# Kernel optimization log

Hardware: AMD Instinct MI355X
Metric: run time of the kernel (lower is better)

## Reference

```python
import jax, jax.numpy as jnp
import numpy as np

N_NODES = 50000
N_EDGES = 640000
HIDDEN = 128
LN_EPS = 1e-5


def setup_inputs() -> dict:
    key = jax.random.key(0)
    k_h, k_e, k_w1, k_w2 = jax.random.split(key, 4)
    s = 1.0 / np.sqrt(HIDDEN)
    return {
        "h": jax.random.normal(k_h, (N_NODES, HIDDEN), dtype=jnp.float32),
        "edge_index": jax.random.randint(k_e, (2, N_EDGES), 0, N_NODES, dtype=jnp.int32),
        "W1": jax.random.normal(k_w1, (HIDDEN, HIDDEN), dtype=jnp.float32) * s,
        "b1": jnp.zeros((HIDDEN,), dtype=jnp.float32),
        "W2": jax.random.normal(k_w2, (HIDDEN, HIDDEN), dtype=jnp.float32) * s,
        "b2": jnp.zeros((HIDDEN,), dtype=jnp.float32),
        "eps": jnp.zeros((), dtype=jnp.float32),  # GINConv train_eps init
        "gamma": jnp.ones((HIDDEN,), dtype=jnp.float32),
        "beta": jnp.zeros((HIDDEN,), dtype=jnp.float32),
    }


def reference(h, edge_index, W1, b1, W2, b2, eps, gamma, beta):
    src, dst = edge_index[0], edge_index[1]
    # GIN aggregation: sum of neighbor features scattered to destination nodes
    agg = jax.ops.segment_sum(h[src], dst, num_segments=h.shape[0])  # (N, D)
    z = (1.0 + eps) * h + agg
    # 2-layer MLP: Linear -> ReLU -> Linear (torch Linear: x @ W.T + b)
    z = jax.nn.relu(z @ W1.T + b1)
    h_conv = z @ W2.T + b2
    # residual + LayerNorm + ReLU (dropout is identity in eval mode)
    h_res = h_conv + h
    mu = jnp.mean(h_res, axis=-1, keepdims=True)
    var = jnp.var(h_res, axis=-1, keepdims=True)
    h_norm = (h_res - mu) * jax.lax.rsqrt(var + LN_EPS) * gamma + beta
    return jax.nn.relu(h_norm)
```

## Files before the change

kernel.cpp:

```cpp
#include <hip/hip_runtime.h>

#define HID 128
#define LN_EPS 1e-5f
#define LDSW 136

typedef __attribute__((ext_vector_type(8))) short bf16x8;
typedef __attribute__((ext_vector_type(4))) float f32x4;

static __device__ __forceinline__ unsigned short f2bf(float f) {
  unsigned int x = __float_as_uint(f);
  x += 0x7fffu + ((x >> 16) & 1u);
  return (unsigned short)(x >> 16);
}
static __device__ __forceinline__ float bflo(unsigned int u) { return __uint_as_float(u << 16); }
static __device__ __forceinline__ float bfhi(unsigned int u) { return __uint_as_float(u & 0xffff0000u); }

__global__ __launch_bounds__(256) void k_count(const int* __restrict__ ei,
                                               int* __restrict__ counts, int nE) {
  const int e = blockIdx.x * 256 + threadIdx.x;
  if (e >= nE) return;
  atomicAdd(&counts[ei[nE + e]], 1);
}

__global__ __launch_bounds__(256) void k_scan1(const int* __restrict__ counts,
                                               int* __restrict__ offsets,
                                               int* __restrict__ bsum, int n) {
  __shared__ int sm[256];
  const int t = threadIdx.x;
  const int i = blockIdx.x * 256 + t;
  const int v = (i < n) ? counts[i] : 0;
  int incl = v;
  sm[t] = incl;
  __syncthreads();
#pragma unroll
  for (int off = 1; off < 256; off <<= 1) {
    const int other = (t >= off) ? sm[t - off] : 0;
    __syncthreads();
    incl += other;
    sm[t] = incl;
    __syncthreads();
  }
  if (i < n) offsets[i] = incl - v;
  if (t == 255) bsum[blockIdx.x] = incl;
}

__global__ __launch_bounds__(256) void k_scan2(const int* __restrict__ bsum,
                                               int* __restrict__ ebase,
                                               int* __restrict__ offsets,
                                               int nb, int n) {
  __shared__ int sm[256];
  const int t = threadIdx.x;
  const int v = (t < nb) ? bsum[t] : 0;
  int incl = v;
  sm[t] = incl;
  __syncthreads();
#pragma unroll
  for (int off = 1; off < 256; off <<= 1) {
    const int other = (t >= off) ? sm[t - off] : 0;
    __syncthreads();
    incl += other;
    sm[t] = incl;
    __syncthreads();
  }
  if (t < nb) ebase[t] = incl - v;
  if (t == 255) offsets[n] = incl;
}

__global__ __launch_bounds__(256) void k_scan3(int* __restrict__ offsets,
                                               int* __restrict__ cursors,
                                               const int* __restrict__ ebase, int n) {
  const int i = blockIdx.x * 256 + threadIdx.x;
  if (i >= n) return;
  const int o = offsets[i] + ebase[blockIdx.x];
  offsets[i] = o;
  cursors[i] = o;
}

__global__ __launch_bounds__(256) void k_bucket(const int* __restrict__ ei,
                                                int* __restrict__ cursors,
                                                int* __restrict__ esrc, int nE) {
  const int e = blockIdx.x * 256 + threadIdx.x;
  if (e >= nE) return;
  const int s = ei[e];
  const int d = ei[nE + e];
  const int pos = atomicAdd(&cursors[d], 1);
  esrc[pos] = s;
}

__global__ __launch_bounds__(256) void k_tobf3(const float* __restrict__ h,
                                               const float* __restrict__ w1,
                                               const float* __restrict__ w2,
                                               uint2* __restrict__ hb,
                                               uint2* __restrict__ w1b,
                                               uint2* __restrict__ w2b,
                                               int nh4, int nw4) {
  const int total = nh4 + 2 * nw4;
  const int stride = gridDim.x * 256;
  for (int i = blockIdx.x * 256 + threadIdx.x; i < total; i += stride) {
    const float* src;
    uint2* dst;
    int off;
    if (i < nh4) { src = h; dst = hb; off = i; }
    else if (i < nh4 + nw4) { src = w1; dst = w1b; off = i - nh4; }
    else { src = w2; dst = w2b; off = i - nh4 - nw4; }
    const float4 v = reinterpret_cast<const float4*>(src)[off];
    uint2 p;
    p.x = (unsigned)f2bf(v.x) | ((unsigned)f2bf(v.y) << 16);
    p.y = (unsigned)f2bf(v.z) | ((unsigned)f2bf(v.w) << 16);
    dst[off] = p;
  }
}

__global__ __launch_bounds__(256) void k_gather(const unsigned short* __restrict__ hbf,
                                                const int* __restrict__ offsets,
                                                const int* __restrict__ esrc,
                                                const float* __restrict__ eps,
                                                unsigned short* __restrict__ zbf, int nNodes) {
  const int gid = blockIdx.x * 256 + threadIdx.x;
  const int node = gid >> 5;
  if (node >= nNodes) return;
  const int col4 = (threadIdx.x & 31) * 4;
  const float c = 1.0f + eps[0];

  const uint2 hv = *reinterpret_cast<const uint2*>(hbf + (size_t)node * HID + col4);
  float a0 = c * bflo(hv.x), a1 = c * bfhi(hv.x);
  float a2 = c * bflo(hv.y), a3 = c * bfhi(hv.y);

  const int beg = offsets[node], end = offsets[node + 1];
  int e = beg;
  for (; e + 1 < end; e += 2) {
    const int s0 = esrc[e], s1 = esrc[e + 1];
    const uint2 v0 = *reinterpret_cast<const uint2*>(hbf + (size_t)s0 * HID + col4);
    const uint2 v1 = *reinterpret_cast<const uint2*>(hbf + (size_t)s1 * HID + col4);
    a0 += bflo(v0.x) + bflo(v1.x);
    a1 += bfhi(v0.x) + bfhi(v1.x);
    a2 += bflo(v0.y) + bflo(v1.y);
    a3 += bfhi(v0.y) + bfhi(v1.y);
  }
  if (e < end) {
    const uint2 v0 = *reinterpret_cast<const uint2*>(hbf + (size_t)esrc[e] * HID + col4);
    a0 += bflo(v0.x); a1 += bfhi(v0.x); a2 += bflo(v0.y); a3 += bfhi(v0.y);
  }
  uint2 o;
  o.x = (unsigned)f2bf(a0) | ((unsigned)f2bf(a1) << 16);
  o.y = (unsigned)f2bf(a2) | ((unsigned)f2bf(a3) << 16);
  *reinterpret_cast<uint2*>(zbf + (size_t)node * HID + col4) = o;
}

__global__ __launch_bounds__(256) void k_mmf(const unsigned short* __restrict__ zbf,
                                             const unsigned short* __restrict__ w1,
                                             const unsigned short* __restrict__ w2,
                                             const float* __restrict__ b1,
                                             const float* __restrict__ b2,
                                             const float* __restrict__ h,
                                             const float* __restrict__ gamma,
                                             const float* __restrict__ beta,
                                             float* __restrict__ out, int nTiles) {
  __shared__ unsigned short yt[4][16][LDSW];
  const int wave = threadIdx.x >> 6;
  const int l = threadIdx.x & 63;
  const int mtile = blockIdx.x * 4 + wave;
  if (mtile >= nTiles) return;
  const int row0 = mtile * 16;
  const int lr = l & 15;
  const int lq = l >> 4;

  bf16x8 a[4];
#pragma unroll
  for (int ks = 0; ks < 4; ++ks)
    a[ks] = *reinterpret_cast<const bf16x8*>(zbf + (size_t)(row0 + lr) * HID + ks * 32 + lq * 8);

  f32x4 acc[8];
#pragma unroll
  for (int nt = 0; nt < 8; ++nt) acc[nt] = (f32x4){0.f, 0.f, 0.f, 0.f};
#pragma unroll
  for (int nt = 0; nt < 8; ++nt) {
    const unsigned short* wb = w1 + (size_t)(nt * 16 + lr) * HID + lq * 8;
#pragma unroll
    for (int ks = 0; ks < 4; ++ks) {
      const bf16x8 b = *reinterpret_cast<const bf16x8*>(wb + ks * 32);
      acc[nt] = __builtin_amdgcn_mfma_f32_16x16x32_bf16(a[ks], b, acc[nt], 0, 0, 0);
    }
  }

#pragma unroll
  for (int nt = 0; nt < 8; ++nt) {
    const int cc = nt * 16 + lr;
    const float bs = b1[cc];
#pragma unroll
    for (int r = 0; r < 4; ++r)
      yt[wave][lq * 4 + r][cc] = f2bf(fmaxf(acc[nt][r] + bs, 0.f));
  }

  bf16x8 a2[4];
#pragma unroll
  for (int ks = 0; ks < 4; ++ks)
    a2[ks] = *reinterpret_cast<const bf16x8*>(&yt[wave][lr][ks * 32 + lq * 8]);

#pragma unroll
  for (int nt = 0; nt < 8; ++nt) acc[nt] = (f32x4){0.f, 0.f, 0.f, 0.f};
#pragma unroll
  for (int nt = 0; nt < 8; ++nt) {
    const unsigned short* wb = w2 + (size_t)(nt * 16 + lr) * HID + lq * 8;
#pragma unroll
    for (int ks = 0; ks < 4; ++ks) {
      const bf16x8 b = *reinterpret_cast<const bf16x8*>(wb + ks * 32);
      acc[nt] = __builtin_amdgcn_mfma_f32_16x16x32_bf16(a2[ks], b, acc[nt], 0, 0, 0);
    }
  }

#pragma unroll
  for (int nt = 0; nt < 8; ++nt) {
    const int cc = nt * 16 + lr;
    const float bs = b2[cc];
#pragma unroll
    for (int r = 0; r < 4; ++r) {
      const int row = row0 + lq * 4 + r;
      acc[nt][r] += bs + h[(size_t)row * HID + cc];
    }
  }

  float mu_[4], rstd_[4];
#pragma unroll
  for (int r = 0; r < 4; ++r) {
    float s = 0.f, ss = 0.f;
#pragma unroll
    for (int nt = 0; nt < 8; ++nt) { const float v = acc[nt][r]; s += v; ss += v * v; }
#pragma unroll
    for (int m = 1; m < 16; m <<= 1) {
      s += __shfl_xor(s, m, 64);
      ss += __shfl_xor(ss, m, 64);
    }
    const float mu = s * (1.f / 128.f);
    const float var = ss * (1.f / 128.f) - mu * mu;
    mu_[r] = mu;
    rstd_[r] = rsqrtf(var + LN_EPS);
  }
#pragma unroll
  for (int nt = 0; nt < 8; ++nt) {
    const int cc = nt * 16 + lr;
    const float g = gamma[cc], be = beta[cc];
#pragma unroll
    for (int r = 0; r < 4; ++r) {
      const int row = row0 + lq * 4 + r;
      const float o = (acc[nt][r] - mu_[r]) * rstd_[r] * g + be;
      out[(size_t)row * HID + cc] = fmaxf(o, 0.f);
    }
  }
}

extern "C" void kernel_launch(void* const* d_in, const int* in_sizes, int n_in,
                              void* d_out, int out_size, void* d_ws, size_t ws_size,
                              hipStream_t stream) {
  const float* h     = (const float*)d_in[0];
  const int*   ei    = (const int*)d_in[1];
  const float* W1    = (const float*)d_in[2];
  const float* b1    = (const float*)d_in[3];
  const float* W2    = (const float*)d_in[4];
  const float* b2    = (const float*)d_in[5];
  const float* eps   = (const float*)d_in[6];
  const float* gamma = (const float*)d_in[7];
  const float* beta  = (const float*)d_in[8];

  const int nNodes = in_sizes[0] / HID;
  const int nE     = in_sizes[1] / 2;
  const int nb     = (nNodes + 255) / 256;

  int* counts  = (int*)d_ws;
  int* offsets = counts + nNodes;
  int* cursors = offsets + nNodes + 1;
  int* bsum    = cursors + nNodes;
  int* ebase   = bsum + nb;
  int* esrc    = counts + 150400;
  unsigned short* hbf  = (unsigned short*)(esrc + nE);
  unsigned short* zbf  = hbf + (size_t)nNodes * HID;
  unsigned short* w1bf = zbf + (size_t)nNodes * HID;
  unsigned short* w2bf = w1bf + HID * HID;

  hipMemsetAsync(counts, 0, (size_t)nNodes * sizeof(int), stream);

  const int eblocks = (nE + 255) / 256;
  k_tobf3<<<2048, 256, 0, stream>>>(h, W1, W2, (uint2*)hbf, (uint2*)w1bf, (uint2*)w2bf,
                                    nNodes * HID / 4, HID * HID / 4);
  k_count<<<eblocks, 256, 0, stream>>>(ei, counts, nE);
  k_scan1<<<nb, 256, 0, stream>>>(counts, offsets, bsum, nNodes);
  k_scan2<<<1, 256, 0, stream>>>(bsum, ebase, offsets, nb, nNodes);
  k_scan3<<<nb, 256, 0, stream>>>(offsets, cursors, ebase, nNodes);
  k_bucket<<<eblocks, 256, 0, stream>>>(ei, cursors, esrc, nE);

  k_gather<<<(nNodes * 32 + 255) / 256, 256, 0, stream>>>(hbf, offsets, esrc, eps, zbf, nNodes);

  const int nTiles = nNodes / 16;
  const int mblocks = (nTiles + 3) / 4;
  k_mmf<<<mblocks, 256, 0, stream>>>(zbf, w1bf, w2bf, b1, b2, h, gamma, beta,
                                     (float*)d_out, nTiles);
}
```

Before: 247.8 us.

## Split MLP output columns across four waves per 16-row tile in fused kernel

The fused MLP+LayerNorm kernel previously gave each wave a full 16-row tile covering all 128 output columns. Now a block handles one 16-row tile, and each of its four waves computes 32 output columns. The hidden activation is shared through LDS, and the LayerNorm partial sums are combined across waves with a block barrier. This gives four times as many blocks and fewer accumulator registers per wave, raising occupancy. In exchange, every wave reloads the same A fragment, two __syncthreads are added, and extra LDS traffic is needed for the reduction.

```diff
diff --git a/kernel.cpp b/kernel.cpp
--- a/kernel.cpp
+++ b/kernel.cpp
@@ -156,10 +156,11 @@
                                              const float* __restrict__ gamma,
                                              const float* __restrict__ beta,
                                              float* __restrict__ out, int nTiles) {
-  __shared__ unsigned short yt[4][16][LDSW];
+  __shared__ unsigned short yt[16][LDSW];
+  __shared__ float lnp[16][4][2];
   const int wave = threadIdx.x >> 6;
   const int l = threadIdx.x & 63;
-  const int mtile = blockIdx.x * 4 + wave;
+  const int mtile = blockIdx.x;
   if (mtile >= nTiles) return;
   const int row0 = mtile * 16;
   const int lr = l & 15;
@@ -170,66 +171,85 @@
   for (int ks = 0; ks < 4; ++ks)
     a[ks] = *reinterpret_cast<const bf16x8*>(zbf + (size_t)(row0 + lr) * HID + ks * 32 + lq * 8);
 
-  f32x4 acc[8];
-#pragma unroll
-  for (int nt = 0; nt < 8; ++nt) acc[nt] = (f32x4){0.f, 0.f, 0.f, 0.f};
-#pragma unroll
-  for (int nt = 0; nt < 8; ++nt) {
+  f32x4 acc[2];
+#pragma unroll
+  for (int j = 0; j < 2; ++j) acc[j] = (f32x4){0.f, 0.f, 0.f, 0.f};
+#pragma unroll
+  for (int j = 0; j < 2; ++j) {
+    const int nt = wave * 2 + j;
     const unsigned short* wb = w1 + (size_t)(nt * 16 + lr) * HID + lq * 8;
 #pragma unroll
     for (int ks = 0; ks < 4; ++ks) {
       const bf16x8 b = *reinterpret_cast<const bf16x8*>(wb + ks * 32);
-      acc[nt] = __builtin_amdgcn_mfma_f32_16x16x32_bf16(a[ks], b, acc[nt], 0, 0, 0);
-    }
-  }
-
-#pragma unroll
-  for (int nt = 0; nt < 8; ++nt) {
-    const int cc = nt * 16 + lr;
+      acc[j] = __builtin_amdgcn_mfma_f32_16x16x32_bf16(a[ks], b, acc[j], 0, 0, 0);
+    }
+  }
+
+#pragma unroll
+  for (int j = 0; j < 2; ++j) {
+    const int cc = (wave * 2 + j) * 16 + lr;
     const float bs = b1[cc];
 #pragma unroll
     for (int r = 0; r < 4; ++r)
-      yt[wave][lq * 4 + r][cc] = f2bf(fmaxf(acc[nt][r] + bs, 0.f));
-  }
+      yt[lq * 4 + r][cc] = f2bf(fmaxf(acc[j][r] + bs, 0.f));
+  }
+  __syncthreads();
 
   bf16x8 a2[4];
 #pragma unroll
   for (int ks = 0; ks < 4; ++ks)
-    a2[ks] = *reinterpret_cast<const bf16x8*>(&yt[wave][lr][ks * 32 + lq * 8]);
-
-#pragma unroll
-  for (int nt = 0; nt < 8; ++nt) acc[nt] = (f32x4){0.f, 0.f, 0.f, 0.f};
-#pragma unroll
-  for (int nt = 0; nt < 8; ++nt) {
+    a2[ks] = *reinterpret_cast<const bf16x8*>(&yt[lr][ks * 32 + lq * 8]);
+
+#pragma unroll
+  for (int j = 0; j < 2; ++j) acc[j] = (f32x4){0.f, 0.f, 0.f, 0.f};
+#pragma unroll
+  for (int j = 0; j < 2; ++j) {
+    const int nt = wave * 2 + j;
     const unsigned short* wb = w2 + (size_t)(nt * 16 + lr) * HID + lq * 8;
 #pragma unroll
     for (int ks = 0; ks < 4; ++ks) {
       const bf16x8 b = *reinterpret_cast<const bf16x8*>(wb + ks * 32);
-      acc[nt] = __builtin_amdgcn_mfma_f32_16x16x32_bf16(a2[ks], b, acc[nt], 0, 0, 0);
-    }
-  }
-
-#pragma unroll
-  for (int nt = 0; nt < 8; ++nt) {
-    const int cc = nt * 16 + lr;
+      acc[j] = __builtin_amdgcn_mfma_f32_16x16x32_bf16(a2[ks], b, acc[j], 0, 0, 0);
+    }
+  }
+
+#pragma unroll
+  for (int j = 0; j < 2; ++j) {
+    const int cc = (wave * 2 + j) * 16 + lr;
     const float bs = b2[cc];
 #pragma unroll
     for (int r = 0; r < 4; ++r) {
       const int row = row0 + lq * 4 + r;
-      acc[nt][r] += bs + h[(size_t)row * HID + cc];
-    }
-  }
-
-  float mu_[4], rstd_[4];
+      acc[j][r] += bs + h[(size_t)row * HID + cc];
+    }
+  }
+
 #pragma unroll
   for (int r = 0; r < 4; ++r) {
-    float s = 0.f, ss = 0.f;
-#pragma unroll
-    for (int nt = 0; nt < 8; ++nt) { const float v = acc[nt][r]; s += v; ss += v * v; }
+    float s = acc[0][r] + acc[1][r];
+    float ss = acc[0][r] * acc[0][r] + acc[1][r] * acc[1][r];
 #pragma unroll
     for (int m = 1; m < 16; m <<= 1) {
       s += __shfl_xor(s, m, 64);
       ss += __shfl_xor(ss, m, 64);
+    }
+    if (lr == 0) {
+      lnp[lq * 4 + r][wave][0] = s;
+      lnp[lq * 4 + r][wave][1] = ss;
+    }
+  }
+  __syncthreads();
+
+  float mu_[4], rstd_[4];
+#pragma unroll
+  for (int r = 0; r < 4; ++r) {
+    const int rt = lq * 4 + r;
+    float s = 0.f, ss = 0.f;
+#pragma unroll
+    for (int w = 0; w < 4; ++w) {
+      const float2 p = *reinterpret_cast<const float2*>(&lnp[rt][w][0]);
+      s += p.x;
+      ss += p.y;
     }
     const float mu = s * (1.f / 128.f);
     const float var = ss * (1.f / 128.f) - mu * mu;
@@ -237,13 +257,13 @@
     rstd_[r] = rsqrtf(var + LN_EPS);
   }
 #pragma unroll
-  for (int nt = 0; nt < 8; ++nt) {
-    const int cc = nt * 16 + lr;
+  for (int j = 0; j < 2; ++j) {
+    const int cc = (wave * 2 + j) * 16 + lr;
     const float g = gamma[cc], be = beta[cc];
 #pragma unroll
     for (int r = 0; r < 4; ++r) {
       const int row = row0 + lq * 4 + r;
-      const float o = (acc[nt][r] - mu_[r]) * rstd_[r] * g + be;
+      const float o = (acc[j][r] - mu_[r]) * rstd_[r] * g + be;
       out[(size_t)row * HID + cc] = fmaxf(o, 0.f);
     }
   }
@@ -291,7 +311,6 @@
   k_gather<<<(nNodes * 32 + 255) / 256, 256, 0, stream>>>(hbf, offsets, esrc, eps, zbf, nNodes);
 
   const int nTiles = nNodes / 16;
-  const int mblocks = (nTiles + 3) / 4;
-  k_mmf<<<mblocks, 256, 0, stream>>>(zbf, w1bf, w2bf, b1, b2, h, gamma, beta,
-                                     (float*)d_out, nTiles);
-}
+  k_mmf<<<nTiles, 256, 0, stream>>>(zbf, w1bf, w2bf, b1, b2, h, gamma, beta,
+                                    (float*)d_out, nTiles);
+}
```

Result: no change. 243.2 us (-1.9%).
